# Optimization experiments

Hardware: AMD Instinct MI355X
Metric: run time of the kernel (lower is better)

The kernel has to match this reference:

```python
import jax, jax.numpy as jnp
import numpy as np
from itertools import product

L_LEVELS = 3
PAD = 2
DN = ('NCH', 'OIH', 'NCH')


def _realign(S, L):
    # Faithful port of SCI_Net.realign(): order of concatenated leaves, then inverse perm.
    out = []
    for comb in product((0, 1), repeat=L):
        v = np.arange(S)
        for b in comb:
            v = v[b::2] if b == 1 else v[::2]
        out.append(v)
    order = np.concatenate(out)          # concat position -> original time index
    return np.argsort(order)             # original-time-sorted positions (row1 of `a`)


def _conv_op(x, w1, w2):
    # ReplicationPad1d -> Conv1d(C->C*e) -> LeakyReLU(0.01) -> Dropout(eval=id) -> Conv1d(C*e->C) -> Tanh
    xp = jnp.pad(x, ((0, 0), (0, 0), (PAD, PAD)), mode='edge')
    h = jax.lax.conv_general_dilated(xp, w1, (1,), 'VALID', dimension_numbers=DN)
    h = jnp.where(h > 0, h, 0.01 * h)
    h = jax.lax.conv_general_dilated(h, w2, (1,), 'VALID', dimension_numbers=DN)
    return jnp.tanh(h)


def setup_inputs() -> dict:
    key = jax.random.key(0)
    ks = jax.random.split(key, 7)
    B, C, S, E, K = 128, 8, 8192, 4, 3
    return {
        'x': jax.random.normal(ks[0], (B, C, S), jnp.float32),
        'conv_w1': jax.random.normal(ks[1], (L_LEVELS, 4, C * E, C, K), jnp.float32) * 0.2,
        'conv_w2': jax.random.normal(ks[2], (L_LEVELS, 4, C, C * E, K), jnp.float32) * 0.1,
        'fc1_w': jax.random.normal(ks[3], (50, S), jnp.float32) * 0.01,
        'fc1_b': jax.random.normal(ks[4], (50,), jnp.float32) * 0.01,
        'fc2_w': jax.random.normal(ks[5], (24, 50), jnp.float32) * 0.1,
        'fc2_b': jax.random.normal(ks[6], (24,), jnp.float32) * 0.01,
    }


def reference(x, conv_w1, conv_w2, fc1_w, fc1_b, fc2_w, fc2_b):
    B, C, S = x.shape
    prev = x[None]  # [n_branch=1, B, C, T]
    for lvl in range(L_LEVELS):
        n, _, _, T = prev.shape
        xb = prev.reshape(n * B, C, T)
        # NOTE: idx_even = arange(1,T,2), idx_odd = arange(0,T,2) in the source.
        F_even = xb[:, :, 1::2]
        F_odd = xb[:, :, 0::2]
        w1, w2 = conv_w1[lvl], conv_w2[lvl]  # op order: 0=nu, 1=psi, 2=ro, 3=phi (shared across branches)
        F_even_s = F_even * jnp.exp(_conv_op(F_odd, w1[1], w2[1]))   # psi
        F_odd_s = F_odd * jnp.exp(_conv_op(F_even, w1[3], w2[3]))    # phi
        F_even_final = F_odd_s - _conv_op(F_odd_s, w1[0], w2[0])     # nu
        F_odd_final = F_even_s + _conv_op(F_even_s, w1[2], w2[2])    # ro
        T2 = T // 2
        new = jnp.stack([F_even_final.reshape(n, B, C, T2),
                         F_odd_final.reshape(n, B, C, T2)], axis=1)  # [n, 2, B, C, T2]
        prev = new.reshape(2 * n, B, C, T2)
    ridx = jnp.asarray(_realign(S, L_LEVELS))
    F_concat = jnp.transpose(prev, (1, 2, 0, 3)).reshape(B, C, S)  # concat leaves on time dim
    F_concat = F_concat[:, :, ridx] + x                            # reverse-index scatter + residual
    h = jax.nn.relu(jnp.einsum('bcs,hs->bch', F_concat, fc1_w) + fc1_b)
    return jnp.einsum('bch,oh->bco', h, fc2_w) + fc2_b  # [B, C, horizon]
```

## Files before the change

### kernel.cpp

```cpp
#include <hip/hip_runtime.h>

#define TT   256
#define TIN2 (TT + 8)
#define NHA  (TT + 6)
#define NEO  (TT + 4)
#define NHB  (TT + 2)

typedef _Float16 h2 __attribute__((ext_vector_type(2)));
typedef __fp16 fp16v2 __attribute__((ext_vector_type(2)));
typedef _Float16 f16x8 __attribute__((ext_vector_type(8)));
typedef float f32x4 __attribute__((ext_vector_type(4)));

__device__ _Float16 g_w1A[12][2][64][8];
__device__ _Float16 g_w2A[12][3][64][8];

__device__ __forceinline__ h2 pkh(float a, float b) {
  fp16v2 r = __builtin_amdgcn_cvt_pkrtz(a, b);
  return __builtin_bit_cast(h2, r);
}
__device__ __forceinline__ unsigned int pku(float a, float b) {
  return __builtin_bit_cast(unsigned int, pkh(a, b));
}
__device__ __forceinline__ float fast_tanh(float x) {
  return 1.f - __fdividef(2.f, __expf(2.f * x) + 1.f);
}
__device__ __forceinline__ unsigned int lky(unsigned int u) {
  h2 v = __builtin_bit_cast(h2, u);
  h2 s = v * (h2){(_Float16)0.01f, (_Float16)0.01f};
  h2 m = __builtin_elementwise_max(v, s);
  return __builtin_bit_cast(unsigned int, m);
}
__device__ __forceinline__ float lane_spread(float a_low, float b_low, int lane) {
  float s = __shfl_xor(b_low, 32);
  return (lane >= 32) ? s : a_low;
}
#define HID_PTR(hid, side, row, g) (&(hid)[side][row][(((g) ^ (((row) >> 1) & 3)) * 8)])

__global__ __launch_bounds__(256) void pack_mfma(
    const float* __restrict__ w1, const float* __restrict__ w2)
{
  int id = blockIdx.x * 256 + threadIdx.x;
  if (id >= 12 * 5 * 64) return;
  const int lane = id & 63;
  const int rest = id >> 6;
  const int slot = rest % 5;
  const int pr   = rest / 5;
  if (slot < 2) {
    const int oc = slot * 16 + (lane & 15);
    const int bb = lane >> 4;
#pragma unroll
    for (int j = 0; j < 8; ++j) {
      float v = (bb < 3) ? w1[((size_t)pr * 32 + oc) * 24 + j * 3 + bb] : 0.f;
      g_w1A[pr][slot][lane][j] = (_Float16)v;
    }
  } else {
    const int t = slot - 2;
    const int oc = lane & 15;
    const int kk = lane >> 4;
#pragma unroll
    for (int j = 0; j < 8; ++j) {
      const int hc = (j < 4) ? (4 * kk + j) : (16 + 4 * kk + (j - 4));
      float v = (oc < 8) ? w2[((size_t)pr * 8 + oc) * 96 + hc * 3 + t] : 0.f;
      g_w2A[pr][t][lane][j] = (_Float16)v;
    }
  }
}

template <bool IN16>
__global__ __launch_bounds__(512) void level_fused(
    const void* __restrict__ Xv, _Float16* __restrict__ NEXT,
    int lvl, int T2, int tilesPerSeq)
{
  __shared__ __align__(16) _Float16 inS[2][TIN2][8];
  __shared__ __align__(16) _Float16 hidS[2][NHA][32];
  __shared__ __align__(16) _Float16 esS[2][NEO][8];

  const int blk = blockIdx.x;
  const int nb  = blk / tilesPerSeq;
  const int t0  = (blk - nb * tilesPerSeq) * TT;

  if constexpr (IN16) {
    const _Float16* Xh = (const _Float16*)Xv + (size_t)nb * (2 * (size_t)T2) * 8;
    for (int it = threadIdx.x; it < 2 * TIN2; it += 512) {
      const int s = it & 1, jj = it >> 1;
      int p = t0 - 4 + jj;
      p = p < 0 ? 0 : (p > T2 - 1 ? T2 - 1 : p);
      *(uint4*)&inS[s][jj][0] = *(const uint4*)&Xh[(size_t)(2 * p + s) * 8];
    }
  } else {
    const float* X = (const float*)Xv;
    const float2* Xrow = (const float2*)(X + (size_t)nb * 8 * (2 * (size_t)T2));
    for (int jj = threadIdx.x; jj < TIN2; jj += 512) {
      int j = t0 - 4 + jj;
      j = j < 0 ? 0 : (j > T2 - 1 ? T2 - 1 : j);
      unsigned int u0[4], u1[4];
#pragma unroll
      for (int cp = 0; cp < 4; ++cp) {
        float2 a = Xrow[(size_t)(2 * cp) * T2 + j];
        float2 b = Xrow[(size_t)(2 * cp + 1) * T2 + j];
        u0[cp] = pku(a.x, b.x);
        u1[cp] = pku(a.y, b.y);
      }
      *(uint4*)&inS[0][jj][0] = make_uint4(u0[0], u0[1], u0[2], u0[3]);
      *(uint4*)&inS[1][jj][0] = make_uint4(u1[0], u1[1], u1[2], u1[3]);
    }
  }
  __syncthreads();

  const int wid  = __builtin_amdgcn_readfirstlane((int)(threadIdx.x >> 6));
  const int lane = threadIdx.x & 63;
  const int side = wid >> 2, q = wid & 3;
  const int g = lane >> 4, col = lane & 15;
  const int tstart = (q == 0) ? 0 : (1 + 4 * q);
  const int tcnt   = (q == 0) ? 5 : 4;
  const int a1cnt  = (q == 3) ? 4 : (tcnt + 1);
  const int rp = ((lane >> 4) & 1) * 2 + (lane >> 5);

  const int pa = lvl * 4 + (side ? 3 : 1);
  const int pb = lvl * 4 + (side ? 2 : 0);
  const f16x8 a1w0 = *(const f16x8*)&g_w1A[pa][0][lane][0];
  const f16x8 a1w1 = *(const f16x8*)&g_w1A[pa][1][lane][0];
  const f16x8 a2w0 = *(const f16x8*)&g_w2A[pa][0][lane][0];
  const f16x8 a2w1 = *(const f16x8*)&g_w2A[pa][1][lane][0];
  const f16x8 a2w2 = *(const f16x8*)&g_w2A[pa][2][lane][0];
  const f16x8 b1w0 = *(const f16x8*)&g_w1A[pb][0][lane][0];
  const f16x8 b1w1 = *(const f16x8*)&g_w1A[pb][1][lane][0];
  const f16x8 b2w0 = *(const f16x8*)&g_w2A[pb][0][lane][0];
  const f16x8 b2w1 = *(const f16x8*)&g_w2A[pb][1][lane][0];
  const f16x8 b2w2 = *(const f16x8*)&g_w2A[pb][2][lane][0];
  const f32x4 zero = {0.f, 0.f, 0.f, 0.f};

#pragma unroll
  for (int nt = 0; nt < 6; ++nt) {
    if (nt >= a1cnt) break;
    const int row = (tstart + nt) * 16 + col;
    const int rr = (row + g > TIN2 - 1) ? (TIN2 - 1) : (row + g);
    const f16x8 bf = *(const f16x8*)&inS[side][rr][0];
    f32x4 d0 = __builtin_amdgcn_mfma_f32_16x16x32_f16(a1w0, bf, zero, 0, 0, 0);
    f32x4 d1 = __builtin_amdgcn_mfma_f32_16x16x32_f16(a1w1, bf, zero, 0, 0, 0);
    if (row < NHA) {
      *(uint4*)HID_PTR(hidS, side, row, g) = make_uint4(
          lky(pku(d0[0], d0[1])), lky(pku(d0[2], d0[3])),
          lky(pku(d1[0], d1[1])), lky(pku(d1[2], d1[3])));
    }
  }

#pragma unroll
  for (int nt = 0; nt < 5; ++nt) {
    if (nt >= tcnt) break;
    const int row = (tstart + nt) * 16 + col;
    f32x4 acc = zero;
    acc = __builtin_amdgcn_mfma_f32_16x16x32_f16(a2w0, *(const f16x8*)HID_PTR(hidS, side, row,     g), acc, 0, 0, 0);
    acc = __builtin_amdgcn_mfma_f32_16x16x32_f16(a2w1, *(const f16x8*)HID_PTR(hidS, side, row + 1, g), acc, 0, 0, 0);
    acc = __builtin_amdgcn_mfma_f32_16x16x32_f16(a2w2, *(const f16x8*)HID_PTR(hidS, side, row + 2, g), acc, 0, 0, 0);
    if (row < NEO) {
      const float va = lane_spread(acc[0], acc[2], lane);
      const float vb = lane_spread(acc[1], acc[3], lane);
      const h2 mpk = *(const h2*)&inS[side ^ 1][row + 2][2 * rp];
      const float v0 = (float)mpk[0] * __expf(fast_tanh(va));
      const float v1 = (float)mpk[1] * __expf(fast_tanh(vb));
      *(unsigned int*)&esS[side][row][2 * rp] = pku(v0, v1);
    }
  }
  __syncthreads();

  const int srcB = side ^ 1;
  const int eoLo = (t0 == 0) ? 2 : 0;
  const int eoHi = (t0 + TT >= T2) ? (TT + 1) : (NEO - 1);
#pragma unroll
  for (int nt = 0; nt < 5; ++nt) {
    const int row = (4 * q + nt) * 16 + col;
    int rr = row + g;
    rr = rr < eoLo ? eoLo : (rr > eoHi ? eoHi : rr);
    const f16x8 bf = *(const f16x8*)&esS[srcB][rr][0];
    f32x4 d0 = __builtin_amdgcn_mfma_f32_16x16x32_f16(b1w0, bf, zero, 0, 0, 0);
    f32x4 d1 = __builtin_amdgcn_mfma_f32_16x16x32_f16(b1w1, bf, zero, 0, 0, 0);
    if (row < NHB) {
      *(uint4*)HID_PTR(hidS, side, row, g) = make_uint4(
          lky(pku(d0[0], d0[1])), lky(pku(d0[2], d0[3])),
          lky(pku(d1[0], d1[1])), lky(pku(d1[2], d1[3])));
    }
  }

  const float sgn = side ? 1.f : -1.f;
  const int i = nb >> 7;
  const int b = nb & 127;
  const int outseq = 2 * i + side;
  _Float16* outbase = NEXT + ((size_t)outseq * 128 + b) * (size_t)T2 * 8;
#pragma unroll
  for (int nt = 0; nt < 4; ++nt) {
    const int row = q * 64 + nt * 16 + col;
    f32x4 acc = zero;
    acc = __builtin_amdgcn_mfma_f32_16x16x32_f16(b2w0, *(const f16x8*)HID_PTR(hidS, side, row,     g), acc, 0, 0, 0);
    acc = __builtin_amdgcn_mfma_f32_16x16x32_f16(b2w1, *(const f16x8*)HID_PTR(hidS, side, row + 1, g), acc, 0, 0, 0);
    acc = __builtin_amdgcn_mfma_f32_16x16x32_f16(b2w2, *(const f16x8*)HID_PTR(hidS, side, row + 2, g), acc, 0, 0, 0);
    const float va = lane_spread(acc[0], acc[2], lane);
    const float vb = lane_spread(acc[1], acc[3], lane);
    const h2 base = *(const h2*)&esS[srcB][row + 2][2 * rp];
    const int tg = t0 + row;
    *(unsigned int*)&outbase[(size_t)tg * 8 + 2 * rp] =
        pku((float)base[0] + sgn * fast_tanh(va), (float)base[1] + sgn * fast_tanh(vb));
  }
}

__global__ __launch_bounds__(256) void fc1_fused(
    const _Float16* __restrict__ P, const float* __restrict__ x,
    const float* __restrict__ W, float* __restrict__ partial)
{
  const int rt = blockIdx.x & 31;
  const int ch = blockIdx.x >> 5;
  const int s0 = ch * 512;
  __shared__ unsigned int Fl[32][68];
  __shared__ unsigned int Wl[64][68];
  const int hg = threadIdx.x & 15;
  const int rg = threadIdx.x >> 4;
  float acc[2][4] = {{0.f, 0.f, 0.f, 0.f}, {0.f, 0.f, 0.f, 0.f}};

  for (int sb = 0; sb < 512; sb += 128) {
    __syncthreads();
    for (int i = threadIdx.x; i < 32 * 32; i += 256) {
      const int r = i >> 5, s4 = i & 31;
      const int row = rt * 32 + r;
      const int b = row >> 3, c = row & 7;
      const int base = s0 + sb + 4 * s4;
      const int t = base >> 3, r0 = base & 7;
      const float4 xv = *(const float4*)(x + (size_t)row * 8192 + base);
      _Float16 p[4];
#pragma unroll
      for (int j = 0; j < 4; ++j) {
        const int rr = r0 + j;
        const int rev = ((rr & 1) << 2) | (rr & 2) | ((rr >> 2) & 1);
        p[j] = P[(((size_t)rev * 128 + b) * 1024 + t) * 8 + c];
      }
      const h2 f01 = pkh(xv.x, xv.y) + (h2){p[0], p[1]};
      const h2 f23 = pkh(xv.z, xv.w) + (h2){p[2], p[3]};
      *(uint2*)&Fl[r][s4 * 2] = make_uint2(__builtin_bit_cast(unsigned int, f01),
                                           __builtin_bit_cast(unsigned int, f23));
    }
    for (int i = threadIdx.x; i < 64 * 32; i += 256) {
      const int hh = i >> 5, s4 = i & 31;
      float4 v = make_float4(0.f, 0.f, 0.f, 0.f);
      if (hh < 50) v = ((const float4*)(W + (size_t)hh * 8192 + s0 + sb))[s4];
      *(uint2*)&Wl[hh][s4 * 2] = make_uint2(pku(v.x, v.y), pku(v.z, v.w));
    }
    __syncthreads();
    for (int q = 0; q < 16; ++q) {
      const uint4 fa = *(const uint4*)&Fl[rg * 2][q * 4];
      const uint4 fb = *(const uint4*)&Fl[rg * 2 + 1][q * 4];
#pragma unroll
      for (int j = 0; j < 4; ++j) {
        const uint4 w = *(const uint4*)&Wl[hg + 16 * j][q * 4];
#pragma unroll
        for (int e = 0; e < 4; ++e) {
          const h2 we = __builtin_bit_cast(h2, (&w.x)[e]);
          acc[0][j] = __builtin_amdgcn_fdot2(we, __builtin_bit_cast(h2, (&fa.x)[e]), acc[0][j], false);
          acc[1][j] = __builtin_amdgcn_fdot2(we, __builtin_bit_cast(h2, (&fb.x)[e]), acc[1][j], false);
        }
      }
    }
  }
#pragma unroll
  for (int rr = 0; rr < 2; ++rr)
#pragma unroll
    for (int j = 0; j < 4; ++j)
      partial[((size_t)ch * 1024 + rt * 32 + rg * 2 + rr) * 64 + hg + 16 * j] = acc[rr][j];
}

__global__ __launch_bounds__(256) void fc_stage2(
    const float* __restrict__ partial, const float* __restrict__ fc1b,
    const float* __restrict__ fc2w, const float* __restrict__ fc2b,
    float* __restrict__ out)
{
  const int rr = threadIdx.x >> 6;
  const int row = blockIdx.x * 4 + rr;
  const int h = threadIdx.x & 63;
  __shared__ float hs[4][64];
  float v = 0.f;
  if (h < 50) {
    for (int ch = 0; ch < 16; ++ch)
      v += partial[((size_t)ch * 1024 + row) * 64 + h];
    v += fc1b[h];
    v = v > 0.f ? v : 0.f;
  }
  hs[rr][h] = v;
  __syncthreads();
  if (h < 24) {
    float a = fc2b[h];
    for (int j = 0; j < 50; ++j)
      a = fmaf(hs[rr][j], fc2w[h * 50 + j], a);
    out[(size_t)row * 24 + h] = a;
  }
}

extern "C" void kernel_launch(void* const* d_in, const int* in_sizes, int n_in,
                              void* d_out, int out_size, void* d_ws, size_t ws_size,
                              hipStream_t stream)
{
  const float* x    = (const float*)d_in[0];
  const float* w1a  = (const float*)d_in[1];
  const float* w2a  = (const float*)d_in[2];
  const float* fc1w = (const float*)d_in[3];
  const float* fc1b = (const float*)d_in[4];
  const float* fc2w = (const float*)d_in[5];
  const float* fc2b = (const float*)d_in[6];
  float* out = (float*)d_out;

  _Float16* bufA = (_Float16*)d_ws;
  _Float16* bufB = bufA + (size_t)9 * 1024 * 1024;
  float* partial = (float*)((char*)d_ws + (size_t)40 * 1024 * 1024);

  pack_mfma<<<dim3(15), dim3(256), 0, stream>>>(w1a, w2a);

  level_fused<false><<<dim3(2048), dim3(512), 0, stream>>>(x,    bufA, 0, 4096, 16);
  level_fused<true ><<<dim3(2048), dim3(512), 0, stream>>>(bufA, bufB, 1, 2048, 8);
  level_fused<true ><<<dim3(2048), dim3(512), 0, stream>>>(bufB, bufA, 2, 1024, 4);

  fc1_fused<<<dim3(512), dim3(256), 0, stream>>>(bufA, x, fc1w, partial);
  fc_stage2<<<dim3(256), dim3(256), 0, stream>>>(partial, fc1b, fc2w, fc2b, out);
  (void)in_sizes; (void)n_in; (void)out_size; (void)ws_size;
}
```

Measured before the change: 119.5 us.

## Share one hidden buffer across sides and process sides sequentially

All eight waves now work on one branch side at a time instead of splitting the waves four per side. This halves the hidden-activation LDS buffer and adds a min-occupancy launch bound, so more blocks can be resident per CU. Weight fragments are loaded per side, so fewer of them stay live in registers at once. The cost is extra block-wide barriers between side passes and some overlapping tiles computed twice by neighbouring waves.

Measured after the change: 127.2 us. 6.5% more time.

```diff
diff --git a/kernel.cpp b/kernel.cpp
--- a/kernel.cpp
+++ b/kernel.cpp
@@ -34,7 +34,7 @@
   float s = __shfl_xor(b_low, 32);
   return (lane >= 32) ? s : a_low;
 }
-#define HID_PTR(hid, side, row, g) (&(hid)[side][row][(((g) ^ (((row) >> 1) & 3)) * 8)])
+#define HID_PTR(row, g) (&hidS[row][(((g) ^ (((row) >> 1) & 3)) * 8)])
 
 __global__ __launch_bounds__(256) void pack_mfma(
     const float* __restrict__ w1, const float* __restrict__ w2)
@@ -67,12 +67,12 @@
 }
 
 template <bool IN16>
-__global__ __launch_bounds__(512) void level_fused(
+__global__ __launch_bounds__(512, 8) void level_fused(
     const void* __restrict__ Xv, _Float16* __restrict__ NEXT,
     int lvl, int T2, int tilesPerSeq)
 {
   __shared__ __align__(16) _Float16 inS[2][TIN2][8];
-  __shared__ __align__(16) _Float16 hidS[2][NHA][32];
+  __shared__ __align__(16) _Float16 hidS[NHA][32];
   __shared__ __align__(16) _Float16 esS[2][NEO][8];
 
   const int blk = blockIdx.x;
@@ -109,97 +109,103 @@
 
   const int wid  = __builtin_amdgcn_readfirstlane((int)(threadIdx.x >> 6));
   const int lane = threadIdx.x & 63;
-  const int side = wid >> 2, q = wid & 3;
   const int g = lane >> 4, col = lane & 15;
-  const int tstart = (q == 0) ? 0 : (1 + 4 * q);
-  const int tcnt   = (q == 0) ? 5 : 4;
-  const int a1cnt  = (q == 3) ? 4 : (tcnt + 1);
+  const int t2 = 2 * wid;
+  const int a2cnt = (wid == 7) ? 3 : 2;
   const int rp = ((lane >> 4) & 1) * 2 + (lane >> 5);
 
-  const int pa = lvl * 4 + (side ? 3 : 1);
-  const int pb = lvl * 4 + (side ? 2 : 0);
-  const f16x8 a1w0 = *(const f16x8*)&g_w1A[pa][0][lane][0];
-  const f16x8 a1w1 = *(const f16x8*)&g_w1A[pa][1][lane][0];
-  const f16x8 a2w0 = *(const f16x8*)&g_w2A[pa][0][lane][0];
-  const f16x8 a2w1 = *(const f16x8*)&g_w2A[pa][1][lane][0];
-  const f16x8 a2w2 = *(const f16x8*)&g_w2A[pa][2][lane][0];
-  const f16x8 b1w0 = *(const f16x8*)&g_w1A[pb][0][lane][0];
-  const f16x8 b1w1 = *(const f16x8*)&g_w1A[pb][1][lane][0];
-  const f16x8 b2w0 = *(const f16x8*)&g_w2A[pb][0][lane][0];
-  const f16x8 b2w1 = *(const f16x8*)&g_w2A[pb][1][lane][0];
-  const f16x8 b2w2 = *(const f16x8*)&g_w2A[pb][2][lane][0];
   const f32x4 zero = {0.f, 0.f, 0.f, 0.f};
-
-#pragma unroll
-  for (int nt = 0; nt < 6; ++nt) {
-    if (nt >= a1cnt) break;
-    const int row = (tstart + nt) * 16 + col;
-    const int rr = (row + g > TIN2 - 1) ? (TIN2 - 1) : (row + g);
-    const f16x8 bf = *(const f16x8*)&inS[side][rr][0];
-    f32x4 d0 = __builtin_amdgcn_mfma_f32_16x16x32_f16(a1w0, bf, zero, 0, 0, 0);
-    f32x4 d1 = __builtin_amdgcn_mfma_f32_16x16x32_f16(a1w1, bf, zero, 0, 0, 0);
-    if (row < NHA) {
-      *(uint4*)HID_PTR(hidS, side, row, g) = make_uint4(
-          lky(pku(d0[0], d0[1])), lky(pku(d0[2], d0[3])),
-          lky(pku(d1[0], d1[1])), lky(pku(d1[2], d1[3])));
-    }
-  }
-
-#pragma unroll
-  for (int nt = 0; nt < 5; ++nt) {
-    if (nt >= tcnt) break;
-    const int row = (tstart + nt) * 16 + col;
-    f32x4 acc = zero;
-    acc = __builtin_amdgcn_mfma_f32_16x16x32_f16(a2w0, *(const f16x8*)HID_PTR(hidS, side, row,     g), acc, 0, 0, 0);
-    acc = __builtin_amdgcn_mfma_f32_16x16x32_f16(a2w1, *(const f16x8*)HID_PTR(hidS, side, row + 1, g), acc, 0, 0, 0);
-    acc = __builtin_amdgcn_mfma_f32_16x16x32_f16(a2w2, *(const f16x8*)HID_PTR(hidS, side, row + 2, g), acc, 0, 0, 0);
-    if (row < NEO) {
+  const int i = nb >> 7;
+  const int b = nb & 127;
+
+#pragma unroll
+  for (int s = 0; s < 2; ++s) {
+    const int pa = lvl * 4 + (s ? 3 : 1);
+    const f16x8 a1w0 = *(const f16x8*)&g_w1A[pa][0][lane][0];
+    const f16x8 a1w1 = *(const f16x8*)&g_w1A[pa][1][lane][0];
+    const f16x8 a2w0 = *(const f16x8*)&g_w2A[pa][0][lane][0];
+    const f16x8 a2w1 = *(const f16x8*)&g_w2A[pa][1][lane][0];
+    const f16x8 a2w2 = *(const f16x8*)&g_w2A[pa][2][lane][0];
+
+#pragma unroll
+    for (int nt = 0; nt < 3; ++nt) {
+      const int row = (t2 + nt) * 16 + col;
+      const int rr = (row + g > TIN2 - 1) ? (TIN2 - 1) : (row + g);
+      const f16x8 bf = *(const f16x8*)&inS[s][rr][0];
+      f32x4 d0 = __builtin_amdgcn_mfma_f32_16x16x32_f16(a1w0, bf, zero, 0, 0, 0);
+      f32x4 d1 = __builtin_amdgcn_mfma_f32_16x16x32_f16(a1w1, bf, zero, 0, 0, 0);
+      if (row < NHA) {
+        *(uint4*)HID_PTR(row, g) = make_uint4(
+            lky(pku(d0[0], d0[1])), lky(pku(d0[2], d0[3])),
+            lky(pku(d1[0], d1[1])), lky(pku(d1[2], d1[3])));
+      }
+    }
+
+#pragma unroll
+    for (int nt = 0; nt < 3; ++nt) {
+      if (nt >= a2cnt) break;
+      const int row = (t2 + nt) * 16 + col;
+      f32x4 acc = zero;
+      acc = __builtin_amdgcn_mfma_f32_16x16x32_f16(a2w0, *(const f16x8*)HID_PTR(row,     g), acc, 0, 0, 0);
+      acc = __builtin_amdgcn_mfma_f32_16x16x32_f16(a2w1, *(const f16x8*)HID_PTR(row + 1, g), acc, 0, 0, 0);
+      acc = __builtin_amdgcn_mfma_f32_16x16x32_f16(a2w2, *(const f16x8*)HID_PTR(row + 2, g), acc, 0, 0, 0);
+      if (row < NEO) {
+        const float va = lane_spread(acc[0], acc[2], lane);
+        const float vb = lane_spread(acc[1], acc[3], lane);
+        const h2 mpk = *(const h2*)&inS[s ^ 1][row + 2][2 * rp];
+        const float v0 = (float)mpk[0] * __expf(fast_tanh(va));
+        const float v1 = (float)mpk[1] * __expf(fast_tanh(vb));
+        *(unsigned int*)&esS[s][row][2 * rp] = pku(v0, v1);
+      }
+    }
+    __syncthreads();
+  }
+
+  const int eoLo = (t0 == 0) ? 2 : 0;
+  const int eoHi = (t0 + TT >= T2) ? (TT + 1) : (NEO - 1);
+#pragma unroll
+  for (int s = 0; s < 2; ++s) {
+    const int pb = lvl * 4 + (s ? 2 : 0);
+    const f16x8 b1w0 = *(const f16x8*)&g_w1A[pb][0][lane][0];
+    const f16x8 b1w1 = *(const f16x8*)&g_w1A[pb][1][lane][0];
+    const f16x8 b2w0 = *(const f16x8*)&g_w2A[pb][0][lane][0];
+    const f16x8 b2w1 = *(const f16x8*)&g_w2A[pb][1][lane][0];
+    const f16x8 b2w2 = *(const f16x8*)&g_w2A[pb][2][lane][0];
+    const int srcB = s ^ 1;
+
+#pragma unroll
+    for (int nt = 0; nt < 3; ++nt) {
+      const int row = (t2 + nt) * 16 + col;
+      int rr = row + g;
+      rr = rr < eoLo ? eoLo : (rr > eoHi ? eoHi : rr);
+      const f16x8 bf = *(const f16x8*)&esS[srcB][rr][0];
+      f32x4 d0 = __builtin_amdgcn_mfma_f32_16x16x32_f16(b1w0, bf, zero, 0, 0, 0);
+      f32x4 d1 = __builtin_amdgcn_mfma_f32_16x16x32_f16(b1w1, bf, zero, 0, 0, 0);
+      if (row < NHB) {
+        *(uint4*)HID_PTR(row, g) = make_uint4(
+            lky(pku(d0[0], d0[1])), lky(pku(d0[2], d0[3])),
+            lky(pku(d1[0], d1[1])), lky(pku(d1[2], d1[3])));
+      }
+    }
+
+    const int outseq = 2 * i + s;
+    const float sgn = s ? 1.f : -1.f;
+    _Float16* outbase = NEXT + ((size_t)outseq * 128 + b) * (size_t)T2 * 8;
+#pragma unroll
+    for (int nt = 0; nt < 2; ++nt) {
+      const int row = (t2 + nt) * 16 + col;
+      f32x4 acc = zero;
+      acc = __builtin_amdgcn_mfma_f32_16x16x32_f16(b2w0, *(const f16x8*)HID_PTR(row,     g), acc, 0, 0, 0);
+      acc = __builtin_amdgcn_mfma_f32_16x16x32_f16(b2w1, *(const f16x8*)HID_PTR(row + 1, g), acc, 0, 0, 0);
+      acc = __builtin_amdgcn_mfma_f32_16x16x32_f16(b2w2, *(const f16x8*)HID_PTR(row + 2, g), acc, 0, 0, 0);
       const float va = lane_spread(acc[0], acc[2], lane);
       const float vb = lane_spread(acc[1], acc[3], lane);
-      const h2 mpk = *(const h2*)&inS[side ^ 1][row + 2][2 * rp];
-      const float v0 = (float)mpk[0] * __expf(fast_tanh(va));
-      const float v1 = (float)mpk[1] * __expf(fast_tanh(vb));
-      *(unsigned int*)&esS[side][row][2 * rp] = pku(v0, v1);
-    }
-  }
-  __syncthreads();
-
-  const int srcB = side ^ 1;
-  const int eoLo = (t0 == 0) ? 2 : 0;
-  const int eoHi = (t0 + TT >= T2) ? (TT + 1) : (NEO - 1);
-#pragma unroll
-  for (int nt = 0; nt < 5; ++nt) {
-    const int row = (4 * q + nt) * 16 + col;
-    int rr = row + g;
-    rr = rr < eoLo ? eoLo : (rr > eoHi ? eoHi : rr);
-    const f16x8 bf = *(const f16x8*)&esS[srcB][rr][0];
-    f32x4 d0 = __builtin_amdgcn_mfma_f32_16x16x32_f16(b1w0, bf, zero, 0, 0, 0);
-    f32x4 d1 = __builtin_amdgcn_mfma_f32_16x16x32_f16(b1w1, bf, zero, 0, 0, 0);
-    if (row < NHB) {
-      *(uint4*)HID_PTR(hidS, side, row, g) = make_uint4(
-          lky(pku(d0[0], d0[1])), lky(pku(d0[2], d0[3])),
-          lky(pku(d1[0], d1[1])), lky(pku(d1[2], d1[3])));
-    }
-  }
-
-  const float sgn = side ? 1.f : -1.f;
-  const int i = nb >> 7;
-  const int b = nb & 127;
-  const int outseq = 2 * i + side;
-  _Float16* outbase = NEXT + ((size_t)outseq * 128 + b) * (size_t)T2 * 8;
-#pragma unroll
-  for (int nt = 0; nt < 4; ++nt) {
-    const int row = q * 64 + nt * 16 + col;
-    f32x4 acc = zero;
-    acc = __builtin_amdgcn_mfma_f32_16x16x32_f16(b2w0, *(const f16x8*)HID_PTR(hidS, side, row,     g), acc, 0, 0, 0);
-    acc = __builtin_amdgcn_mfma_f32_16x16x32_f16(b2w1, *(const f16x8*)HID_PTR(hidS, side, row + 1, g), acc, 0, 0, 0);
-    acc = __builtin_amdgcn_mfma_f32_16x16x32_f16(b2w2, *(const f16x8*)HID_PTR(hidS, side, row + 2, g), acc, 0, 0, 0);
-    const float va = lane_spread(acc[0], acc[2], lane);
-    const float vb = lane_spread(acc[1], acc[3], lane);
-    const h2 base = *(const h2*)&esS[srcB][row + 2][2 * rp];
-    const int tg = t0 + row;
-    *(unsigned int*)&outbase[(size_t)tg * 8 + 2 * rp] =
-        pku((float)base[0] + sgn * fast_tanh(va), (float)base[1] + sgn * fast_tanh(vb));
+      const h2 base = *(const h2*)&esS[srcB][row + 2][2 * rp];
+      const int tg = t0 + row;
+      *(unsigned int*)&outbase[(size_t)tg * 8 + 2 * rp] =
+          pku((float)base[0] + sgn * fast_tanh(va), (float)base[1] + sgn * fast_tanh(vb));
+    }
+    if (s == 0) __syncthreads();
   }
 }
 
```
